# Optimization experiments

Measured on AMD Instinct MI355X. Metric: run time of the kernel, lower is better.

## Reference

```python
import jax, jax.numpy as jnp
import numpy as np

NUM_THINGS = 80
NUM_STUFF = 53
IGNORE_CLASS = NUM_THINGS + NUM_STUFF  # 133, default ignore_class == -1 path
OVERLAP_THR = 0.5
STUFF_AREA_THR = 4096
THING_CONF_THR = 0.5
INSTANCE_OFFSET = 1000
NUM_SEM_CLASSES = NUM_THINGS + NUM_STUFF + 1  # label range [0, 133]


def setup_inputs() -> dict:
    key = jax.random.key(0)
    k1, k2, k3, k4 = jax.random.split(key, 4)
    B, N, H, W = 2, 100, 800, 1344
    ins_masks = jax.random.randint(k1, (B, N, H, W), 0, 2).astype(jnp.bool_)
    ins_scores = jax.random.uniform(k2, (B, N), dtype=jnp.float32)
    ins_class_ids = jax.random.randint(k3, (B, N), 0, NUM_THINGS, dtype=jnp.int32)
    sem_masks = jax.random.randint(k4, (B, H, W), 0, NUM_SEM_CLASSES, dtype=jnp.int32)
    return {"ins_masks": ins_masks, "ins_scores": ins_scores,
            "ins_class_ids": ins_class_ids, "sem_masks": sem_masks}


def _combine_segms(masks, scores, cls_ids, sem):
    # masks: [N,H,W] bool, scores: [N] f32, cls_ids: [N] i32, sem: [H,W] i32
    order = jnp.argsort(-scores)  # descending by score
    masks = masks[order]
    scores = scores[order]
    cls_ids = cls_ids[order]

    def step(carry, xs):
        pan, iid = carry  # pan: [H,W] i32, iid: i32 (next instance id)
        m, s, c = xs
        area = jnp.sum(m).astype(jnp.float32)
        inter = jnp.sum(m & (pan != 0)).astype(jnp.float32)
        keep = (s >= THING_CONF_THR) & (area > 0) & (inter <= OVERLAP_THR * area)
        write = keep & m & (pan == 0)  # only overwrite free pixels
        pan = jnp.where(write, c + iid * INSTANCE_OFFSET, pan)
        iid = iid + keep.astype(jnp.int32)
        return (pan, iid), None

    pan0 = jnp.zeros(masks.shape[1:], dtype=jnp.int32)
    (pan, _), _ = jax.lax.scan(step, (pan0, jnp.int32(1)), (masks, scores, cls_ids))

    # Stuff fusion: pixels claimed by things become ignore class, then any
    # remaining semantic class with area >= thr (and not ignored) is written.
    sem2 = jnp.where(pan > 0, IGNORE_CLASS, sem)
    counts = jnp.zeros((NUM_SEM_CLASSES,), jnp.int32).at[sem2.ravel()].add(1)
    valid = counts >= STUFF_AREA_THR
    valid = valid.at[IGNORE_CLASS].set(False)
    pan = jnp.where(valid[sem2], sem2 + NUM_THINGS, pan)
    return pan


def reference(ins_masks, ins_scores, ins_class_ids, sem_masks):
    # Batched greedy panoptic fusion -> [B,H,W] int32
    return jax.vmap(_combine_segms)(ins_masks, ins_scores, ins_class_ids, sem_masks)
```

## Files before the change

kernel.cpp:

```cpp
#include <hip/hip_runtime.h>
#include <stdint.h>

#define NB 2
#define NN 100
#define HWP (800*1344)
#define GCH 10
#define NCHMAX 10
#define NKEY (1<<(GCH+1))
#define CBIT (1u<<GCH)
#define NSEM 134
#define IGN 133
#define THR 1024
#define BPI 128
#define GRID (NB*BPI)
#define PPB (HWP/BPI)
#define GPX 8
#define NG (PPB/GPX)

struct WS {
  unsigned hist[NCHMAX][NB][NKEY];
  unsigned counts[NB][NSEM];
  int      iid[NB][NN];
  int      order[NB][NN];
  float    score_s[NB][NN];
  int      cls_s[NB][NN];
  unsigned kcAfter[NCHMAX][NB];
  unsigned Mcnt[NB];
  unsigned flag;
};
#define ZW (NCHMAX*NB*NKEY + NB*NSEM + NB*NN)

__device__ __forceinline__ unsigned u8x8_to_bits(uint2 v) {
  unsigned lo = (((v.x & 0x01010101u) * 0x01020408u) >> 24) & 0xFu;
  unsigned hi = (((v.y & 0x01010101u) * 0x01020408u) >> 24) & 0xFu;
  return lo | (hi << 4);
}

__global__ __launch_bounds__(THR) void k0_setup(
    const void* __restrict__ masks, const float* __restrict__ scores,
    const int* __restrict__ cls, WS* __restrict__ ws, uint8_t* __restrict__ owner) {
  const int t = threadIdx.x, gid = blockIdx.x;
  unsigned tg = (unsigned)gid * THR + t;
  if (tg < (unsigned)ZW) (&ws->hist[0][0][0])[tg] = 0;
  uint4* ow = (uint4*)owner;
  const unsigned nw = (unsigned)(NB * HWP / 16);
  for (unsigned i = tg; i < nw; i += (unsigned)GRID * THR)
    ow[i] = make_uint4(~0u, ~0u, ~0u, ~0u);
  if (gid == 0) {
    __shared__ float ss[NB * NN];
    __shared__ unsigned shDet;
    const unsigned* mw = (const unsigned*)masks;
    unsigned any = 0;
    for (int i = t; i < 4096; i += THR) any |= (mw[i] > 1u) ? 1u : 0u;
    if (t == 0) shDet = 0;
    if (t < NB * NN) ss[t] = scores[t];
    if (t < NB) ws->Mcnt[t] = 0;
    __syncthreads();
    if (any) atomicOr(&shDet, 1u);
    __syncthreads();
    if (t == 0) ws->flag = shDet;
    if (t < NB * NN) {
      int bb = t / NN, i = t % NN;
      float s = ss[bb * NN + i];
      if (s >= 0.5f) {
        int r = 0;
        for (int j = 0; j < NN; ++j) {
          float sj = ss[bb * NN + j];
          if (sj >= 0.5f && (sj > s || (sj == s && j < i))) r++;
        }
        ws->order[bb][r]   = i;
        ws->score_s[bb][r] = s;
        ws->cls_s[bb][r]   = cls[bb * NN + i];
        atomicAdd(&ws->Mcnt[bb], 1u);
      }
    }
  }
}

__global__ __launch_bounds__(THR, 4) void k_chunk(
    const void* __restrict__ masks, const int* __restrict__ sem,
    WS* __restrict__ ws, uint8_t* __restrict__ owner, uint16_t* __restrict__ memb,
    int c, int doHist, int doCounts) {
  __shared__ unsigned lh[NKEY];
  __shared__ int midx[GCH];
  __shared__ unsigned sh_kmask;
  const int t = threadIdx.x, gid = blockIdx.x;
  const int b = gid / BPI, bx = gid % BPI;
  const int M = (int)ws->Mcnt[b];
  int Lp = (c > 0) ? (M - (c - 1) * GCH) : 0; if (Lp > GCH) Lp = GCH;
  int Lc = doHist ? (M - c * GCH) : 0;        if (Lc > GCH) Lc = GCH;
  if (!doCounts && Lp <= 0 && Lc <= 0) return;

  unsigned kmask = 0;
  if (Lp > 0) {
    for (int i = t; i < NKEY; i += THR) lh[i] = ws->hist[c - 1][b][i];
    __syncthreads();
    if (t < 64) {
      unsigned km = 0;
      unsigned kc = (c >= 2) ? ws->kcAfter[c - 2][b] : 0u;
      for (int g = 0; g < Lp; ++g) {
        unsigned sel = km & ((1u << g) - 1u);
        unsigned area = 0, inter = 0;
        for (int i = t; i < NKEY; i += 64) {
          unsigned h = lh[i];
          if (h && (((unsigned)i >> g) & 1u)) {
            area += h;
            if (((unsigned)i >> GCH) | ((unsigned)i & sel)) inter += h;
          }
        }
        #pragma unroll
        for (int off = 32; off; off >>= 1) {
          area  += __shfl_xor(area, off);
          inter += __shfl_xor(inter, off);
        }
        float s = ws->score_s[b][(c - 1) * GCH + g];
        bool keep = (s >= 0.5f) && (area > 0u) && (2u * inter <= area);
        if (keep) {
          km |= 1u << g; kc += 1u;
          if (t == 0 && bx == 0) ws->iid[b][(c - 1) * GCH + g] = (int)kc;
        }
      }
      if (t == 0) { sh_kmask = km; if (bx == 0) ws->kcAfter[c - 1][b] = kc; }
    }
    __syncthreads();
    kmask = sh_kmask;
  }

  if (Lc > 0) {
    for (int i = t; i < NKEY; i += THR) lh[i] = 0;
    if (t < GCH) midx[t] = ws->order[b][(t < Lc) ? (c * GCH + t) : (c * GCH)];
  } else if (doCounts) {
    for (int i = t; i < NSEM; i += THR) lh[i] = 0;
  }
  __syncthreads();

  const int mode_u8 = (int)ws->flag;
  const size_t sbase = (size_t)b * HWP + (size_t)bx * PPB;
  const unsigned lm = (Lc >= GCH) ? (CBIT - 1u) : ((Lc > 0) ? ((1u << Lc) - 1u) : 0u);
  int midx_r[GCH];
  if (Lc > 0) {
    #pragma unroll
    for (int g = 0; g < GCH; ++g) midx_r[g] = __builtin_amdgcn_readfirstlane(midx[g]);
  }

  for (int s = 0; s < 2; ++s) {
    int gr = s * THR + t;
    if (gr >= NG) break;
    int l0 = gr * GPX;
    uint2 ov = *(const uint2*)(owner + sbase + l0);
    unsigned w2[2] = {ov.x, ov.y};
    if (kmask) {
      uint4 mo = *(const uint4*)(memb + sbase + l0);
      unsigned mw[4] = {mo.x, mo.y, mo.z, mo.w};
      bool chg = false;
      #pragma unroll
      for (int k = 0; k < GPX; ++k) {
        unsigned by = (w2[k >> 2] >> ((k & 3) * 8)) & 0xFFu;
        if (by == 0xFFu) {
          unsigned hit = (mw[k >> 1] >> ((k & 1) * 16)) & kmask;
          if (hit) {
            unsigned nb = (unsigned)((c - 1) * GCH + __builtin_ctz(hit));
            w2[k >> 2] = (w2[k >> 2] & ~(0xFFu << ((k & 3) * 8))) | (nb << ((k & 3) * 8));
            chg = true;
          }
        }
      }
      if (chg) *(uint2*)(owner + sbase + l0) = make_uint2(w2[0], w2[1]);
    }
    if (Lc > 0) {
      unsigned key[GPX];
      #pragma unroll
      for (int k = 0; k < GPX; ++k) {
        unsigned by = (w2[k >> 2] >> ((k & 3) * 8)) & 0xFFu;
        key[k] = (by != 0xFFu) ? CBIT : 0u;
      }
      if (mode_u8) {
        #pragma unroll
        for (int g = 0; g < GCH; ++g) {
          const uint8_t* mp = (const uint8_t*)masks +
              (size_t)(b * NN + midx_r[g]) * HWP + (size_t)bx * PPB + l0;
          unsigned b8 = u8x8_to_bits(*(const uint2*)mp);
          #pragma unroll
          for (int k = 0; k < GPX; ++k) key[k] |= ((b8 >> k) & 1u) << g;
        }
      } else {
        #pragma unroll 2
        for (int g = 0; g < GCH; ++g) {
          const uint4* mp = (const uint4*)((const int*)masks +
              (size_t)(b * NN + midx_r[g]) * HWP + (size_t)bx * PPB + l0);
          uint4 a = mp[0], bq = mp[1];
          unsigned b8 = (a.x & 1u) | ((a.y & 1u) << 1) | ((a.z & 1u) << 2) |
                        ((a.w & 1u) << 3) | ((bq.x & 1u) << 4) | ((bq.y & 1u) << 5) |
                        ((bq.z & 1u) << 6) | ((bq.w & 1u) << 7);
          #pragma unroll
          for (int k = 0; k < GPX; ++k) key[k] |= ((b8 >> k) & 1u) << g;
        }
      }
      unsigned fk[GPX];
      #pragma unroll
      for (int k = 0; k < GPX; ++k) fk[k] = key[k] & (lm | CBIT);
      uint4 pk;
      pk.x = fk[0] | (fk[1] << 16); pk.y = fk[2] | (fk[3] << 16);
      pk.z = fk[4] | (fk[5] << 16); pk.w = fk[6] | (fk[7] << 16);
      *(uint4*)(memb + sbase + l0) = pk;
      #pragma unroll
      for (int k = 0; k < GPX; ++k) atomicAdd(&lh[fk[k]], 1u);
    }
    if (doCounts) {
      const uint4* sp = (const uint4*)(sem + sbase + l0);
      uint4 sv0 = sp[0], sv1 = sp[1];
      unsigned sarr[8] = {sv0.x, sv0.y, sv0.z, sv0.w, sv1.x, sv1.y, sv1.z, sv1.w};
      #pragma unroll
      for (int k = 0; k < GPX; ++k) {
        unsigned by = (w2[k >> 2] >> ((k & 3) * 8)) & 0xFFu;
        if (by == 0xFFu && sarr[k] != (unsigned)IGN) atomicAdd(&lh[sarr[k]], 1u);
      }
    }
  }
  __syncthreads();
  if (Lc > 0) {
    for (int i = t; i < NKEY; i += THR) {
      unsigned v = lh[i];
      if (v) atomicAdd(&ws->hist[c][b][i], v);
    }
  } else if (doCounts) {
    for (int i = t; i < NSEM; i += THR) {
      unsigned v = lh[i];
      if (v) atomicAdd(&ws->counts[b][i], v);
    }
  }
}

__global__ __launch_bounds__(THR) void k_writepan(
    const int* __restrict__ sem, const uint8_t* __restrict__ owner,
    const WS* __restrict__ ws, int* __restrict__ out) {
  __shared__ int pval[NN];
  __shared__ int sval[NSEM];
  const int t = threadIdx.x, gid = blockIdx.x;
  const int b = gid / BPI, bx = gid % BPI;
  const size_t sbase = (size_t)b * HWP + (size_t)bx * PPB;
  if (t < NN)  pval[t] = ws->cls_s[b][t] + ws->iid[b][t] * 1000;
  if (t < NSEM) sval[t] = (t != IGN && ws->counts[b][t] >= 4096u) ? (t + 80) : 0;
  __syncthreads();
  for (int s = 0; s < 2; ++s) {
    int gr = s * THR + t;
    if (gr >= NG) break;
    int l0 = gr * GPX;
    uint2 ov = *(const uint2*)(owner + sbase + l0);
    unsigned w2[2] = {ov.x, ov.y};
    const uint4* sp = (const uint4*)(sem + sbase + l0);
    uint4 sv0 = sp[0], sv1 = sp[1];
    unsigned sarr[8] = {sv0.x, sv0.y, sv0.z, sv0.w, sv1.x, sv1.y, sv1.z, sv1.w};
    int4* op = (int4*)(out + sbase + l0);
    #pragma unroll
    for (int q = 0; q < 2; ++q) {
      int res[4];
      #pragma unroll
      for (int j = 0; j < 4; ++j) {
        int k = q * 4 + j;
        unsigned by = (w2[k >> 2] >> ((k & 3) * 8)) & 0xFFu;
        res[j] = (by != 0xFFu) ? pval[by] : sval[sarr[k]];
      }
      op[q] = make_int4(res[0], res[1], res[2], res[3]);
    }
  }
}

extern "C" void kernel_launch(void* const* d_in, const int* in_sizes, int n_in,
                              void* d_out, int out_size, void* d_ws, size_t ws_size,
                              hipStream_t stream) {
  const void*  masks  = d_in[0];
  const float* scores = (const float*)d_in[1];
  const int*   cls    = (const int*)d_in[2];
  const int*   sem    = (const int*)d_in[3];
  int* out = (int*)d_out;

  uint8_t* base = (uint8_t*)d_ws;
  WS* ws = (WS*)base;
  size_t off = (sizeof(WS) + 255) & ~(size_t)255;
  uint8_t*  owner = base + off;
  size_t ob = ((size_t)NB * HWP + 255) & ~(size_t)255;
  uint16_t* memb  = (uint16_t*)(base + off + ob);

  hipLaunchKernelGGL(k0_setup, dim3(GRID), dim3(THR), 0, stream,
                     masks, scores, cls, ws, owner);
  for (int c = 0; c < NCHMAX; ++c)
    hipLaunchKernelGGL(k_chunk, dim3(GRID), dim3(THR), 0, stream,
                       masks, sem, ws, owner, memb, c, 1, 0);
  hipLaunchKernelGGL(k_chunk, dim3(GRID), dim3(THR), 0, stream,
                     masks, sem, ws, owner, memb, NCHMAX, 0, 1);
  hipLaunchKernelGGL(k_writepan, dim3(GRID), dim3(THR), 0, stream,
                     sem, owner, ws, out);
}
```

Baseline: 188.5 us.

## Compute mask area and claimed overlap via popcounts, drop claimed bit from histogram

Per-instance area and overlap with already-claimed pixels are now gathered with per-thread popcount counters, reduced by warp shuffles and written to new workspace arrays. Because of this the claimed-pixel bit is no longer part of the histogram key, so the group size grows from 10 to 11 instances within the same 2048-entry table. Claimed pixels and zero keys no longer issue shared-memory atomics, and fully claimed pixel groups skip the membership store. The cost is extra per-group popcounts and reductions, plus reliance on 16-bit packed counters not overflowing within a block.

```diff
diff --git a/kernel.cpp b/kernel.cpp
--- a/kernel.cpp
+++ b/kernel.cpp
@@ -4,10 +4,9 @@
 #define NB 2
 #define NN 100
 #define HWP (800*1344)
-#define GCH 10
+#define GCH 11
 #define NCHMAX 10
-#define NKEY (1<<(GCH+1))
-#define CBIT (1u<<GCH)
+#define NKEY (1<<GCH)
 #define NSEM 134
 #define IGN 133
 #define THR 1024
@@ -19,6 +18,8 @@
 
 struct WS {
   unsigned hist[NCHMAX][NB][NKEY];
+  unsigned areaA[NCHMAX][NB][GCH];
+  unsigned interC[NCHMAX][NB][GCH];
   unsigned counts[NB][NSEM];
   int      iid[NB][NN];
   int      order[NB][NN];
@@ -28,7 +29,7 @@
   unsigned Mcnt[NB];
   unsigned flag;
 };
-#define ZW (NCHMAX*NB*NKEY + NB*NSEM + NB*NN)
+#define ZW (NCHMAX*NB*NKEY + NCHMAX*NB*GCH*2 + NB*NSEM + NB*NN)
 
 __device__ __forceinline__ unsigned u8x8_to_bits(uint2 v) {
   unsigned lo = (((v.x & 0x01010101u) * 0x01020408u) >> 24) & 0xFu;
@@ -82,6 +83,7 @@
     WS* __restrict__ ws, uint8_t* __restrict__ owner, uint16_t* __restrict__ memb,
     int c, int doHist, int doCounts) {
   __shared__ unsigned lh[NKEY];
+  __shared__ unsigned lhP[GCH];
   __shared__ int midx[GCH];
   __shared__ unsigned sh_kmask;
   const int t = threadIdx.x, gid = blockIdx.x;
@@ -100,19 +102,15 @@
       unsigned kc = (c >= 2) ? ws->kcAfter[c - 2][b] : 0u;
       for (int g = 0; g < Lp; ++g) {
         unsigned sel = km & ((1u << g) - 1u);
-        unsigned area = 0, inter = 0;
+        unsigned interU = 0;
         for (int i = t; i < NKEY; i += 64) {
           unsigned h = lh[i];
-          if (h && (((unsigned)i >> g) & 1u)) {
-            area += h;
-            if (((unsigned)i >> GCH) | ((unsigned)i & sel)) inter += h;
-          }
+          if (h && (((unsigned)i >> g) & 1u) && ((unsigned)i & sel)) interU += h;
         }
         #pragma unroll
-        for (int off = 32; off; off >>= 1) {
-          area  += __shfl_xor(area, off);
-          inter += __shfl_xor(inter, off);
-        }
+        for (int off = 32; off; off >>= 1) interU += __shfl_xor(interU, off);
+        unsigned area  = ws->areaA[c - 1][b][g];
+        unsigned inter = ws->interC[c - 1][b][g] + interU;
         float s = ws->score_s[b][(c - 1) * GCH + g];
         bool keep = (s >= 0.5f) && (area > 0u) && (2u * inter <= area);
         if (keep) {
@@ -128,7 +126,10 @@
 
   if (Lc > 0) {
     for (int i = t; i < NKEY; i += THR) lh[i] = 0;
-    if (t < GCH) midx[t] = ws->order[b][(t < Lc) ? (c * GCH + t) : (c * GCH)];
+    if (t < GCH) {
+      lhP[t] = 0;
+      midx[t] = ws->order[b][(t < Lc) ? (c * GCH + t) : (c * GCH)];
+    }
   } else if (doCounts) {
     for (int i = t; i < NSEM; i += THR) lh[i] = 0;
   }
@@ -136,12 +137,14 @@
 
   const int mode_u8 = (int)ws->flag;
   const size_t sbase = (size_t)b * HWP + (size_t)bx * PPB;
-  const unsigned lm = (Lc >= GCH) ? (CBIT - 1u) : ((Lc > 0) ? ((1u << Lc) - 1u) : 0u);
   int midx_r[GCH];
   if (Lc > 0) {
     #pragma unroll
     for (int g = 0; g < GCH; ++g) midx_r[g] = __builtin_amdgcn_readfirstlane(midx[g]);
   }
+  unsigned cnt[GCH];
+  #pragma unroll
+  for (int g = 0; g < GCH; ++g) cnt[g] = 0;
 
   for (int s = 0; s < 2; ++s) {
     int gr = s * THR + t;
@@ -167,44 +170,56 @@
       }
       if (chg) *(uint2*)(owner + sbase + l0) = make_uint2(w2[0], w2[1]);
     }
+    unsigned claimed8 = 0;
+    #pragma unroll
+    for (int k = 0; k < GPX; ++k)
+      if (((w2[k >> 2] >> ((k & 3) * 8)) & 0xFFu) != 0xFFu) claimed8 |= 1u << k;
+
     if (Lc > 0) {
       unsigned key[GPX];
       #pragma unroll
-      for (int k = 0; k < GPX; ++k) {
-        unsigned by = (w2[k >> 2] >> ((k & 3) * 8)) & 0xFFu;
-        key[k] = (by != 0xFFu) ? CBIT : 0u;
-      }
+      for (int k = 0; k < GPX; ++k) key[k] = 0;
       if (mode_u8) {
         #pragma unroll
         for (int g = 0; g < GCH; ++g) {
-          const uint8_t* mp = (const uint8_t*)masks +
-              (size_t)(b * NN + midx_r[g]) * HWP + (size_t)bx * PPB + l0;
-          unsigned b8 = u8x8_to_bits(*(const uint2*)mp);
-          #pragma unroll
-          for (int k = 0; k < GPX; ++k) key[k] |= ((b8 >> k) & 1u) << g;
+          if (g < Lc) {
+            const uint8_t* mp = (const uint8_t*)masks +
+                (size_t)(b * NN + midx_r[g]) * HWP + (size_t)bx * PPB + l0;
+            unsigned b8 = u8x8_to_bits(*(const uint2*)mp);
+            cnt[g] += __popc(b8) | (__popc(b8 & claimed8) << 16);
+            #pragma unroll
+            for (int k = 0; k < GPX; ++k) key[k] |= ((b8 >> k) & 1u) << g;
+          }
         }
       } else {
         #pragma unroll 2
         for (int g = 0; g < GCH; ++g) {
-          const uint4* mp = (const uint4*)((const int*)masks +
-              (size_t)(b * NN + midx_r[g]) * HWP + (size_t)bx * PPB + l0);
-          uint4 a = mp[0], bq = mp[1];
-          unsigned b8 = (a.x & 1u) | ((a.y & 1u) << 1) | ((a.z & 1u) << 2) |
-                        ((a.w & 1u) << 3) | ((bq.x & 1u) << 4) | ((bq.y & 1u) << 5) |
-                        ((bq.z & 1u) << 6) | ((bq.w & 1u) << 7);
-          #pragma unroll
-          for (int k = 0; k < GPX; ++k) key[k] |= ((b8 >> k) & 1u) << g;
-        }
-      }
-      unsigned fk[GPX];
-      #pragma unroll
-      for (int k = 0; k < GPX; ++k) fk[k] = key[k] & (lm | CBIT);
-      uint4 pk;
-      pk.x = fk[0] | (fk[1] << 16); pk.y = fk[2] | (fk[3] << 16);
-      pk.z = fk[4] | (fk[5] << 16); pk.w = fk[6] | (fk[7] << 16);
-      *(uint4*)(memb + sbase + l0) = pk;
-      #pragma unroll
-      for (int k = 0; k < GPX; ++k) atomicAdd(&lh[fk[k]], 1u);
+          if (g < Lc) {
+            const uint4* mp = (const uint4*)((const int*)masks +
+                (size_t)(b * NN + midx_r[g]) * HWP + (size_t)bx * PPB + l0);
+            uint4 a = mp[0], bq = mp[1];
+            unsigned b8 = (a.x & 1u) | ((a.y & 1u) << 1) | ((a.z & 1u) << 2) |
+                          ((a.w & 1u) << 3) | ((bq.x & 1u) << 4) | ((bq.y & 1u) << 5) |
+                          ((bq.z & 1u) << 6) | ((bq.w & 1u) << 7);
+            cnt[g] += __popc(b8) | (__popc(b8 & claimed8) << 16);
+            #pragma unroll
+            for (int k = 0; k < GPX; ++k) key[k] |= ((b8 >> k) & 1u) << g;
+          }
+        }
+      }
+      if (claimed8 != 0xFFu) {
+        uint4 pk;
+        pk.x = key[0] | (key[1] << 16); pk.y = key[2] | (key[3] << 16);
+        pk.z = key[4] | (key[5] << 16); pk.w = key[6] | (key[7] << 16);
+        *(uint4*)(memb + sbase + l0) = pk;
+        #pragma unroll
+        for (int k = 0; k < GPX; ++k) {
+          if (!((claimed8 >> k) & 1u)) {
+            unsigned fk = key[k];
+            if (fk) atomicAdd(&lh[fk], 1u);
+          }
+        }
+      }
     }
     if (doCounts) {
       const uint4* sp = (const uint4*)(sem + sbase + l0);
@@ -212,16 +227,29 @@
       unsigned sarr[8] = {sv0.x, sv0.y, sv0.z, sv0.w, sv1.x, sv1.y, sv1.z, sv1.w};
       #pragma unroll
       for (int k = 0; k < GPX; ++k) {
-        unsigned by = (w2[k >> 2] >> ((k & 3) * 8)) & 0xFFu;
-        if (by == 0xFFu && sarr[k] != (unsigned)IGN) atomicAdd(&lh[sarr[k]], 1u);
+        if (!((claimed8 >> k) & 1u) && sarr[k] != (unsigned)IGN)
+          atomicAdd(&lh[sarr[k]], 1u);
       }
     }
   }
   __syncthreads();
   if (Lc > 0) {
+    #pragma unroll
+    for (int g = 0; g < GCH; ++g) {
+      unsigned v = cnt[g];
+      #pragma unroll
+      for (int off = 32; off; off >>= 1) v += __shfl_xor(v, off);
+      if ((t & 63) == 0 && v) atomicAdd(&lhP[g], v);
+    }
+    __syncthreads();
     for (int i = t; i < NKEY; i += THR) {
       unsigned v = lh[i];
       if (v) atomicAdd(&ws->hist[c][b][i], v);
+    }
+    if (t < GCH && t < Lc) {
+      unsigned p = lhP[t];
+      if (p & 0xFFFFu) atomicAdd(&ws->areaA[c][b][t], p & 0xFFFFu);
+      if (p >> 16)     atomicAdd(&ws->interC[c][b][t], p >> 16);
     }
   } else if (doCounts) {
     for (int i = t; i < NSEM; i += THR) {
```

New measurement: 220.4 us. +16.9%, slower.

## Drop membership buffer; re-read prior-chunk masks for owner update

Applied to the files above, without the earlier changes.

Removes the 16-bit per-pixel membership buffer that stored each chunk's mask bits for the next pass. The owner update now re-reads the previous chunk's kept masks directly, stopping once all 8 pixels in a group are claimed. The previous chunk's histogram is kept in registers instead of being staged through shared memory, which removes a barrier. For c<=1 the owner load is skipped. This trades a buffer write and read per pixel for up to ten extra mask reads per kept instance, which may hit cache.

```diff
diff --git a/kernel.cpp b/kernel.cpp
--- a/kernel.cpp
+++ b/kernel.cpp
@@ -34,6 +34,15 @@
   unsigned lo = (((v.x & 0x01010101u) * 0x01020408u) >> 24) & 0xFu;
   unsigned hi = (((v.y & 0x01010101u) * 0x01020408u) >> 24) & 0xFu;
   return lo | (hi << 4);
+}
+
+__device__ __forceinline__ unsigned load8(const void* __restrict__ masks,
+                                          size_t eo, int mode_u8) {
+  if (mode_u8) return u8x8_to_bits(*(const uint2*)((const uint8_t*)masks + eo));
+  const uint4* mp = (const uint4*)((const int*)masks + eo);
+  uint4 a = mp[0], b = mp[1];
+  return (a.x & 1u) | ((a.y & 1u) << 1) | ((a.z & 1u) << 2) | ((a.w & 1u) << 3) |
+         ((b.x & 1u) << 4) | ((b.y & 1u) << 5) | ((b.z & 1u) << 6) | ((b.w & 1u) << 7);
 }
 
 __global__ __launch_bounds__(THR) void k0_setup(
@@ -79,10 +88,11 @@
 
 __global__ __launch_bounds__(THR, 4) void k_chunk(
     const void* __restrict__ masks, const int* __restrict__ sem,
-    WS* __restrict__ ws, uint8_t* __restrict__ owner, uint16_t* __restrict__ memb,
+    WS* __restrict__ ws, uint8_t* __restrict__ owner,
     int c, int doHist, int doCounts) {
   __shared__ unsigned lh[NKEY];
   __shared__ int midx[GCH];
+  __shared__ int pmidx[GCH];
   __shared__ unsigned sh_kmask;
   const int t = threadIdx.x, gid = blockIdx.x;
   const int b = gid / BPI, bx = gid % BPI;
@@ -91,21 +101,24 @@
   int Lc = doHist ? (M - c * GCH) : 0;        if (Lc > GCH) Lc = GCH;
   if (!doCounts && Lp <= 0 && Lc <= 0) return;
 
-  unsigned kmask = 0;
   if (Lp > 0) {
-    for (int i = t; i < NKEY; i += THR) lh[i] = ws->hist[c - 1][b][i];
-    __syncthreads();
+    if (t < GCH) pmidx[t] = ws->order[b][(c - 1) * GCH + t];
     if (t < 64) {
+      const unsigned* __restrict__ hp = &ws->hist[c - 1][b][0];
+      unsigned h[32];
+      #pragma unroll
+      for (int j = 0; j < 32; ++j) h[j] = hp[t + (j << 6)];
       unsigned km = 0;
       unsigned kc = (c >= 2) ? ws->kcAfter[c - 2][b] : 0u;
       for (int g = 0; g < Lp; ++g) {
         unsigned sel = km & ((1u << g) - 1u);
         unsigned area = 0, inter = 0;
-        for (int i = t; i < NKEY; i += 64) {
-          unsigned h = lh[i];
-          if (h && (((unsigned)i >> g) & 1u)) {
-            area += h;
-            if (((unsigned)i >> GCH) | ((unsigned)i & sel)) inter += h;
+        #pragma unroll
+        for (int j = 0; j < 32; ++j) {
+          unsigned i = (unsigned)t + ((unsigned)j << 6);
+          if ((i >> g) & 1u) {
+            area += h[j];
+            if ((i >> GCH) | (i & sel)) inter += h[j];
           }
         }
         #pragma unroll
@@ -122,9 +135,7 @@
       }
       if (t == 0) { sh_kmask = km; if (bx == 0) ws->kcAfter[c - 1][b] = kc; }
     }
-    __syncthreads();
-    kmask = sh_kmask;
-  }
+  } else if (t == 0) sh_kmask = 0;
 
   if (Lc > 0) {
     for (int i = t; i < NKEY; i += THR) lh[i] = 0;
@@ -134,87 +145,91 @@
   }
   __syncthreads();
 
+  const unsigned kmask = sh_kmask;
   const int mode_u8 = (int)ws->flag;
   const size_t sbase = (size_t)b * HWP + (size_t)bx * PPB;
   const unsigned lm = (Lc >= GCH) ? (CBIT - 1u) : ((Lc > 0) ? ((1u << Lc) - 1u) : 0u);
-  int midx_r[GCH];
+  int midx_r[GCH], pmidx_r[GCH];
   if (Lc > 0) {
     #pragma unroll
     for (int g = 0; g < GCH; ++g) midx_r[g] = __builtin_amdgcn_readfirstlane(midx[g]);
   }
+  if (kmask) {
+    #pragma unroll
+    for (int g = 0; g < GCH; ++g) pmidx_r[g] = __builtin_amdgcn_readfirstlane(pmidx[g]);
+  }
 
   for (int s = 0; s < 2; ++s) {
     int gr = s * THR + t;
     if (gr >= NG) break;
-    int l0 = gr * GPX;
-    uint2 ov = *(const uint2*)(owner + sbase + l0);
-    unsigned w2[2] = {ov.x, ov.y};
+    const int l0 = gr * GPX;
+    const size_t off = (size_t)bx * PPB + l0;
+    unsigned w2[2];
+    unsigned free8;
+    if (c <= 1) {
+      w2[0] = ~0u; w2[1] = ~0u; free8 = 0xFFu;
+    } else {
+      uint2 ov = *(const uint2*)(owner + sbase + l0);
+      w2[0] = ov.x; w2[1] = ov.y;
+      free8 = 0;
+      #pragma unroll
+      for (int k = 0; k < GPX; ++k)
+        if (((w2[k >> 2] >> ((k & 3) * 8)) & 0xFFu) == 0xFFu) free8 |= 1u << k;
+    }
     if (kmask) {
-      uint4 mo = *(const uint4*)(memb + sbase + l0);
-      unsigned mw[4] = {mo.x, mo.y, mo.z, mo.w};
+      unsigned rem = kmask;
       bool chg = false;
-      #pragma unroll
-      for (int k = 0; k < GPX; ++k) {
-        unsigned by = (w2[k >> 2] >> ((k & 3) * 8)) & 0xFFu;
-        if (by == 0xFFu) {
-          unsigned hit = (mw[k >> 1] >> ((k & 1) * 16)) & kmask;
-          if (hit) {
-            unsigned nb = (unsigned)((c - 1) * GCH + __builtin_ctz(hit));
-            w2[k >> 2] = (w2[k >> 2] & ~(0xFFu << ((k & 3) * 8))) | (nb << ((k & 3) * 8));
-            chg = true;
-          }
+      while (rem && free8) {
+        int g = __builtin_ctz(rem); rem &= rem - 1u;
+        unsigned b8 = load8(masks, (size_t)(b * NN + pmidx_r[g]) * HWP + off, mode_u8);
+        unsigned take = b8 & free8;
+        if (take) {
+          unsigned rank = (unsigned)((c - 1) * GCH + g);
+          #pragma unroll
+          for (int k = 0; k < GPX; ++k)
+            if ((take >> k) & 1u)
+              w2[k >> 2] = (w2[k >> 2] & ~(0xFFu << ((k & 3) * 8))) |
+                           (rank << ((k & 3) * 8));
+          free8 &= ~take; chg = true;
         }
       }
       if (chg) *(uint2*)(owner + sbase + l0) = make_uint2(w2[0], w2[1]);
     }
+    const unsigned claimed8 = ~free8 & 0xFFu;
+
     if (Lc > 0) {
       unsigned key[GPX];
       #pragma unroll
-      for (int k = 0; k < GPX; ++k) {
-        unsigned by = (w2[k >> 2] >> ((k & 3) * 8)) & 0xFFu;
-        key[k] = (by != 0xFFu) ? CBIT : 0u;
-      }
+      for (int k = 0; k < GPX; ++k)
+        key[k] = ((claimed8 >> k) & 1u) << GCH;
       if (mode_u8) {
         #pragma unroll
         for (int g = 0; g < GCH; ++g) {
-          const uint8_t* mp = (const uint8_t*)masks +
-              (size_t)(b * NN + midx_r[g]) * HWP + (size_t)bx * PPB + l0;
-          unsigned b8 = u8x8_to_bits(*(const uint2*)mp);
+          unsigned b8 = u8x8_to_bits(*(const uint2*)((const uint8_t*)masks +
+              (size_t)(b * NN + midx_r[g]) * HWP + off));
           #pragma unroll
           for (int k = 0; k < GPX; ++k) key[k] |= ((b8 >> k) & 1u) << g;
         }
       } else {
         #pragma unroll 2
         for (int g = 0; g < GCH; ++g) {
-          const uint4* mp = (const uint4*)((const int*)masks +
-              (size_t)(b * NN + midx_r[g]) * HWP + (size_t)bx * PPB + l0);
-          uint4 a = mp[0], bq = mp[1];
-          unsigned b8 = (a.x & 1u) | ((a.y & 1u) << 1) | ((a.z & 1u) << 2) |
-                        ((a.w & 1u) << 3) | ((bq.x & 1u) << 4) | ((bq.y & 1u) << 5) |
-                        ((bq.z & 1u) << 6) | ((bq.w & 1u) << 7);
+          unsigned b8 = load8(masks, (size_t)(b * NN + midx_r[g]) * HWP + off, 0);
           #pragma unroll
           for (int k = 0; k < GPX; ++k) key[k] |= ((b8 >> k) & 1u) << g;
         }
       }
-      unsigned fk[GPX];
-      #pragma unroll
-      for (int k = 0; k < GPX; ++k) fk[k] = key[k] & (lm | CBIT);
-      uint4 pk;
-      pk.x = fk[0] | (fk[1] << 16); pk.y = fk[2] | (fk[3] << 16);
-      pk.z = fk[4] | (fk[5] << 16); pk.w = fk[6] | (fk[7] << 16);
-      *(uint4*)(memb + sbase + l0) = pk;
-      #pragma unroll
-      for (int k = 0; k < GPX; ++k) atomicAdd(&lh[fk[k]], 1u);
+      #pragma unroll
+      for (int k = 0; k < GPX; ++k)
+        atomicAdd(&lh[key[k] & (lm | CBIT)], 1u);
     }
     if (doCounts) {
       const uint4* sp = (const uint4*)(sem + sbase + l0);
       uint4 sv0 = sp[0], sv1 = sp[1];
       unsigned sarr[8] = {sv0.x, sv0.y, sv0.z, sv0.w, sv1.x, sv1.y, sv1.z, sv1.w};
       #pragma unroll
-      for (int k = 0; k < GPX; ++k) {
-        unsigned by = (w2[k >> 2] >> ((k & 3) * 8)) & 0xFFu;
-        if (by == 0xFFu && sarr[k] != (unsigned)IGN) atomicAdd(&lh[sarr[k]], 1u);
-      }
+      for (int k = 0; k < GPX; ++k)
+        if (((free8 >> k) & 1u) && sarr[k] != (unsigned)IGN)
+          atomicAdd(&lh[sarr[k]], 1u);
     }
   }
   __syncthreads();
@@ -278,17 +293,15 @@
   uint8_t* base = (uint8_t*)d_ws;
   WS* ws = (WS*)base;
   size_t off = (sizeof(WS) + 255) & ~(size_t)255;
-  uint8_t*  owner = base + off;
-  size_t ob = ((size_t)NB * HWP + 255) & ~(size_t)255;
-  uint16_t* memb  = (uint16_t*)(base + off + ob);
+  uint8_t* owner = base + off;
 
   hipLaunchKernelGGL(k0_setup, dim3(GRID), dim3(THR), 0, stream,
                      masks, scores, cls, ws, owner);
   for (int c = 0; c < NCHMAX; ++c)
     hipLaunchKernelGGL(k_chunk, dim3(GRID), dim3(THR), 0, stream,
-                       masks, sem, ws, owner, memb, c, 1, 0);
+                       masks, sem, ws, owner, c, 1, 0);
   hipLaunchKernelGGL(k_chunk, dim3(GRID), dim3(THR), 0, stream,
-                     masks, sem, ws, owner, memb, NCHMAX, 0, 1);
+                     masks, sem, ws, owner, NCHMAX, 0, 1);
   hipLaunchKernelGGL(k_writepan, dim3(GRID), dim3(THR), 0, stream,
                      sem, owner, ws, out);
 }
```

New measurement: 178.5 us. 1.06x faster.
